# Kernel tuning notes

Measured on AMD Instinct MI355X. Metric: run time of the kernel, lower is better.

The kernel has to match this reference:

```python
import jax, jax.numpy as jnp
import numpy as np

B, L = 16, 2048          # batch, raw history length
H, S, M = 512, 8, 512    # hidden_dim, sequence_count, max_seq_len
V = 32000                # shared embed_tokens vocab
TG = 64                  # TIME_GAP_BUCKET_COUNT
LN_EPS = 1e-5


def setup_inputs() -> dict:
    key = jax.random.key(0)
    ks = jax.random.split(key, 16)
    f = lambda k, shp, scale=0.02: jax.random.normal(k, shp, jnp.float32) * scale
    return {
        "history_tokens": jax.random.randint(ks[0], (B, L), 0, V),
        "history_post_tokens": jax.random.randint(ks[1], (B, L), 0, V),
        "history_author_tokens": jax.random.randint(ks[2], (B, L), 0, V),
        "history_action_tokens": jax.random.randint(ks[3], (B, L), 0, V),
        "history_time_gap": jax.random.randint(ks[4], (B, L), 0, TG + 1),
        "history_group_ids": jax.random.randint(ks[5], (B, L), 0, S + 1),
        "history_mask": jax.random.randint(ks[6], (B, L), 0, 2).astype(bool),
        "embed_table": f(ks[7], (V, H)),
        "time_gap_table": f(ks[8], (TG + 1, H)).at[0].set(0.0),   # padding_idx=0
        "seq_id_table": f(ks[9], (S + 1, H)).at[0].set(0.0),      # padding_idx=0
        "pos_table": f(ks[10], (M, H)),
        "ln_gamma": jnp.ones((5 * H,), jnp.float32),
        "ln_beta": jnp.zeros((5 * H,), jnp.float32),
        "w1": f(ks[11], (5 * H, 4 * H)),
        "b1": jnp.zeros((4 * H,), jnp.float32),
        "w2": f(ks[12], (4 * H, H)),
        "b2": jnp.zeros((H,), jnp.float32),
        "empty_tokens": f(ks[13], (S, H)),
    }


def _forward(embed_table, time_gap_table, seq_id_table, pos_table, ln_gamma, ln_beta,
             w1, b1, w2, b2, empty_tokens,
             history_tokens, history_post_tokens, history_author_tokens,
             history_action_tokens, history_time_gap, history_group_ids, history_mask):
    # --- event feature construction: 4 shared-vocab lookups + time-gap embedding ---
    h = embed_table[history_tokens]            # [B,L,H]
    p = embed_table[history_post_tokens]
    a = embed_table[history_author_tokens]
    act = embed_table[history_action_tokens]
    gap_idx = jnp.clip(history_time_gap, 0, TG)
    gap = time_gap_table[gap_idx] * (gap_idx != 0)[..., None]  # padding_idx=0 -> zero vec
    x = jnp.concatenate([h, p, a, act, gap], axis=-1)           # [B,L,5H]

    # --- event_projection: LayerNorm -> Linear -> SiLU -> (Dropout eval) -> Linear ---
    mu = x.mean(-1, keepdims=True)
    var = x.var(-1, keepdims=True)
    xn = (x - mu) * jax.lax.rsqrt(var + LN_EPS) * ln_gamma + ln_beta
    mid = jax.nn.silu(xn @ w1 + b1)                             # [B,L,4H]
    event = mid @ w2 + b2                                       # [B,L,H]

    # --- ragged regroup: for each (b, s) gather masked positions with group id s+1,
    #     keep the LAST M of them, scatter to slots 0..count-1 ---
    gid = history_group_ids                                     # [B,L]
    match = history_mask[:, None, :] & (gid[:, None, :] == jnp.arange(1, S + 1)[None, :, None])  # [B,S,L]
    cum = jnp.cumsum(match.astype(jnp.int32), axis=-1)          # rank+1 within group
    count = cum[..., -1]                                        # [B,S]
    offset = jnp.maximum(count - M, 0)                          # drop all but last M
    slot = cum - 1 - offset[..., None]                          # [B,S,L]
    keep = match & (slot >= 0)
    slot = jnp.where(keep, slot, M)                             # M is out-of-range -> dropped

    b_idx = jnp.arange(B)[:, None, None]
    s_idx = jnp.arange(S)[None, :, None]
    states = jnp.zeros((B, S, M, H), event.dtype)
    states = states.at[b_idx, s_idx, slot].set(event[:, None, :, :], mode="drop")
    smask = jnp.zeros((B, S, M), bool)
    smask = smask.at[b_idx, s_idx, slot].set(True, mode="drop")

    # empty groups get the learned empty token at slot 0
    empty = count == 0                                          # [B,S]
    states = states.at[:, :, 0, :].set(
        jnp.where(empty[..., None], empty_tokens[None], states[:, :, 0, :]))
    smask = smask.at[:, :, 0].set(smask[:, :, 0] | empty)

    # positional + sequence-id embeddings, then zero padded slots
    pos = pos_table[None, None]                                 # [1,1,M,H]
    sid = seq_id_table[1:S + 1][None, :, None, :]               # [1,S,1,H]
    states = (states + pos + sid) * smask[..., None].astype(states.dtype)
    return states, smask


def reference(history_tokens, history_post_tokens, history_author_tokens,
              history_action_tokens, history_time_gap, history_group_ids, history_mask,
              embed_table, time_gap_table, seq_id_table, pos_table, ln_gamma, ln_beta,
              w1, b1, w2, b2, empty_tokens):
    return _forward(embed_table, time_gap_table, seq_id_table, pos_table, ln_gamma, ln_beta,
                    w1, b1, w2, b2, empty_tokens,
                    history_tokens, history_post_tokens, history_author_tokens,
                    history_action_tokens, history_time_gap, history_group_ids, history_mask)
```

## Files before the change

kernel.cpp:

```cpp
#include <hip/hip_runtime.h>
#include <hip/hip_bf16.h>
#include <stdint.h>

#define B_ 16
#define L_ 2048
#define H_ 512
#define S_ 8
#define M_ 512
#define TG_ 64
#define NTOK (B_ * L_)
#define FIVEH (5 * H_)
#define FOURH (4 * H_)

typedef __attribute__((ext_vector_type(4))) float f32x4;
typedef __attribute__((ext_vector_type(8))) short bf16x8;

__device__ __forceinline__ short f2bf(float f) {
  unsigned u = __builtin_bit_cast(unsigned, f);
  unsigned r = (u + 0x7FFFu + ((u >> 16) & 1u)) >> 16;
  return (short)r;
}

__device__ __forceinline__ void gload_lds16(const void* g, void* l) {
  __builtin_amdgcn_global_load_lds(
      (const __attribute__((address_space(1))) unsigned int*)g,
      (__attribute__((address_space(3))) unsigned int*)l, 16, 0, 0);
}


#define BAR __builtin_amdgcn_s_barrier()
#define LGKM0 do { asm volatile("s_waitcnt lgkmcnt(0)" ::: "memory"); \
                   __builtin_amdgcn_sched_barrier(0); } while (0)
#define VMW(n) asm volatile("s_waitcnt vmcnt(" #n ")" ::: "memory")
#define PRIO(p) __builtin_amdgcn_s_setprio(p)

#define STAGE(src, isB, slot, half, kt) do {                                  \
    const short* _s = (src) + (size_t)((half) * 128) * K + (kt);              \
    const int _o = ((isB) ? 65536 : 0) + (slot) * 32768 + (half) * 16384;     \
    gload_lds16(_s + (size_t)sr0 * K + sc0, lds + _o + db0);                  \
    gload_lds16(_s + (size_t)sr1 * K + sc1, lds + _o + db1);                  \
  } while (0)

#define LDA(qr, slot) do { const int _b = (slot) * 32768 + aW + (qr) * 8192;  \
    _Pragma("unroll") for (int fm = 0; fm < 4; ++fm)                          \
    _Pragma("unroll") for (int ks = 0; ks < 2; ++ks)                          \
      a[fm][ks] = *(const bf16x8*)(lds + _b + sA[fm][ks]); } while (0)

#define LDB(dst, qc, slot) do { const int _b = (slot) * 32768 + bW + (qc) * 4096; \
    _Pragma("unroll") for (int fn = 0; fn < 2; ++fn)                          \
    _Pragma("unroll") for (int ks = 0; ks < 2; ++ks)                          \
      dst[fn][ks] = *(const bf16x8*)(lds + _b + sB[fn][ks]); } while (0)

#define MFMA16(qr, qc, bs) do {                                               \
    _Pragma("unroll") for (int fm = 0; fm < 4; ++fm)                          \
    _Pragma("unroll") for (int fn = 0; fn < 2; ++fn)                          \
    _Pragma("unroll") for (int ks = 0; ks < 2; ++ks)                          \
      acc[(qr)*4+fm][(qc)*2+fn] = __builtin_amdgcn_mfma_f32_16x16x32_bf16(    \
          a[fm][ks], bs[fn][ks], acc[(qr)*4+fm][(qc)*2+fn], 0, 0, 0); } while (0)

template<int K>
__device__ __forceinline__ void gemm_core(const short* __restrict__ Ag,
                                          const short* __restrict__ Bg,
                                          char* lds, f32x4 (&acc)[8][4],
                                          int tid) {
  constexpr int NITER = K / 128;
  const int lane = tid & 63;
  const int wave = tid >> 6;
  const int wm = wave >> 2;
  const int wn = wave & 3;
  const int la = lane & 15;
  const int hi = lane >> 4;

  const int x = (la & 7) << 4;
  int sA[4][2], sB[2][2];
#pragma unroll
  for (int fm = 0; fm < 4; ++fm)
#pragma unroll
    for (int ks = 0; ks < 2; ++ks)
      sA[fm][ks] = (((fm * 16 + la) * 128) + (ks * 32 + hi * 8) * 2) ^ x;
#pragma unroll
  for (int fn = 0; fn < 2; ++fn)
#pragma unroll
    for (int ks = 0; ks < 2; ++ks)
      sB[fn][ks] = ((((wn & 1) * 64 + fn * 16 + la) * 128) + (ks * 32 + hi * 8) * 2) ^ x;
  const int aW = wm * 16384;
  const int bW = 65536 + (wn >> 1) * 16384;

  const int db0 = tid * 16, db1 = tid * 16 + 8192;
  const int lb0 = db0 ^ (((db0 >> 7) & 7) << 4);
  const int lb1 = db1 ^ (((db1 >> 7) & 7) << 4);
  const int sr0 = lb0 >> 7, sc0 = (lb0 & 127) >> 1;
  const int sr1 = lb1 >> 7, sc1 = (lb1 & 127) >> 1;

  bf16x8 a[4][2], b0v[2][2], b1v[2][2];

  STAGE(Bg, 1, 0, 0, 0); STAGE(Bg, 1, 0, 1, 0);
  STAGE(Ag, 0, 0, 0, 0); STAGE(Ag, 0, 0, 1, 0);
  STAGE(Bg, 1, 1, 0, 64); STAGE(Bg, 1, 1, 1, 64);
  VMW(0);
  BAR;

  for (int i = 0; i < NITER - 1; ++i) {
    const int kt1 = (2 * i + 1) * 64, kt2 = kt1 + 64, kt3 = kt1 + 128;
    LDA(0, 0); LDB(b0v, 0, 0); STAGE(Ag, 0, 1, 0, kt1);
    BAR; LGKM0; PRIO(1); MFMA16(0, 0, b0v); PRIO(0); BAR;
    LDB(b1v, 1, 0); STAGE(Ag, 0, 1, 1, kt1);
    BAR; LGKM0; PRIO(1); MFMA16(0, 1, b1v); PRIO(0); BAR;
    LDA(1, 0); STAGE(Bg, 1, 0, 0, kt2);
    BAR; LGKM0; PRIO(1); MFMA16(1, 1, b1v); PRIO(0); BAR;
    STAGE(Bg, 1, 0, 1, kt2);
    BAR; LGKM0; PRIO(1); MFMA16(1, 0, b0v); PRIO(0); VMW(4); BAR;
    LDA(0, 1); LDB(b0v, 0, 1); STAGE(Ag, 0, 0, 0, kt2);
    BAR; LGKM0; PRIO(1); MFMA16(0, 0, b0v); PRIO(0); BAR;
    LDB(b1v, 1, 1); STAGE(Ag, 0, 0, 1, kt2);
    BAR; LGKM0; PRIO(1); MFMA16(0, 1, b1v); PRIO(0); BAR;
    LDA(1, 1); STAGE(Bg, 1, 1, 0, kt3);
    BAR; LGKM0; PRIO(1); MFMA16(1, 1, b1v); PRIO(0); BAR;
    STAGE(Bg, 1, 1, 1, kt3);
    BAR; LGKM0; PRIO(1); MFMA16(1, 0, b0v); PRIO(0); VMW(4); BAR;
  }
  {
    const int kt1 = (2 * (NITER - 1) + 1) * 64;
    LDA(0, 0); LDB(b0v, 0, 0); STAGE(Ag, 0, 1, 0, kt1);
    BAR; LGKM0; PRIO(1); MFMA16(0, 0, b0v); PRIO(0); BAR;
    LDB(b1v, 1, 0); STAGE(Ag, 0, 1, 1, kt1);
    BAR; LGKM0; PRIO(1); MFMA16(0, 1, b1v); PRIO(0); BAR;
    LDA(1, 0);
    BAR; LGKM0; PRIO(1); MFMA16(1, 1, b1v); PRIO(0); BAR;
    BAR; LGKM0; PRIO(1); MFMA16(1, 0, b0v); PRIO(0); VMW(0); BAR;
    LDA(0, 1); LDB(b0v, 0, 1);
    BAR; LGKM0; PRIO(1); MFMA16(0, 0, b0v); PRIO(0); BAR;
    LDB(b1v, 1, 1);
    BAR; LGKM0; PRIO(1); MFMA16(0, 1, b1v); PRIO(0); BAR;
    LDA(1, 1);
    BAR; LGKM0; PRIO(1); MFMA16(1, 1, b1v); PRIO(0); BAR;
    BAR; LGKM0; PRIO(1); MFMA16(1, 0, b0v); PRIO(0);
  }
}

__global__ __launch_bounds__(512, 2) void gemm1_kernel(
    const short* __restrict__ A, const short* __restrict__ Bt,
    const float* __restrict__ bias, const int* __restrict__ nkeep,
    short* __restrict__ C) {
  const int bn = blockIdx.x & 7;
  const int bm = blockIdx.x >> 3;
  if (bm * 256 >= nkeep[0]) return;
  __shared__ __align__(16) char lds[131072];
  const int tid = threadIdx.x;
  f32x4 acc[8][4] = {};
  gemm_core<FIVEH>(A + (size_t)bm * 256 * FIVEH, Bt + (size_t)bn * 256 * FIVEH,
                   lds, acc, tid);
  const int lane = tid & 63, wave = tid >> 6;
  const int wm = wave >> 2, wn = wave & 3;
  const int la = lane & 15, hi = lane >> 4;
  const int row0 = bm * 256 + wm * 128 + hi * 4;
  const int col0 = bn * 256 + wn * 64 + la;
#pragma unroll
  for (int mi = 0; mi < 8; ++mi)
#pragma unroll
    for (int ni = 0; ni < 4; ++ni) {
      const int col = col0 + ni * 16;
      const float bv = bias[col];
#pragma unroll
      for (int r = 0; r < 4; ++r) {
        const int row = row0 + mi * 16 + r;
        float v = acc[mi][ni][r] + bv;
        float sg = 1.f / (1.f + __expf(-v));
        C[(size_t)row * FOURH + col] = f2bf(v * sg);
      }
    }
}

__global__ __launch_bounds__(512, 2) void gemm2_kernel(
    const short* __restrict__ A, const short* __restrict__ Bt,
    const float* __restrict__ b2, const float* __restrict__ pos,
    const float* __restrict__ sidtab, const int* __restrict__ destv,
    const int* __restrict__ nkeep, float* __restrict__ states) {
  const int bn = blockIdx.x & 1;
  const int bm = blockIdx.x >> 1;
  const int nk = nkeep[0];
  if (bm * 256 >= nk) return;
  __shared__ __align__(16) char lds[131072];
  const int tid = threadIdx.x;
  f32x4 acc[8][4] = {};
  gemm_core<FOURH>(A + (size_t)bm * 256 * FOURH, Bt + (size_t)bn * 256 * FOURH,
                   lds, acc, tid);
  const int lane = tid & 63, wave = tid >> 6;
  const int wm = wave >> 2, wn = wave & 3;
  const int la = lane & 15, hi = lane >> 4;
  const int row0 = bm * 256 + wm * 128 + hi * 4;
  const int col0 = bn * 256 + wn * 64 + la;
#pragma unroll
  for (int mi = 0; mi < 8; ++mi) {
#pragma unroll
    for (int r = 0; r < 4; ++r) {
      const int row = row0 + mi * 16 + r;
      if (row >= nk) continue;
      const int dest = destv[row];
      const int slot = dest & (M_ - 1);
      const int gs = dest >> 9;
      const int s = gs & (S_ - 1);
      float* orow = states + (size_t)dest * H_;
#pragma unroll
      for (int n = 0; n < 4; ++n) {
        const int col = col0 + n * 16;
        orow[col] = acc[mi][n][r] + b2[col] + pos[slot * H_ + col] +
                    sidtab[(s + 1) * H_ + col];
      }
    }
  }
}

__global__ __launch_bounds__(256) void transpose_cvt_kernel(
    const float* __restrict__ in, short* __restrict__ out, int K, int N) {
  __shared__ float tile[32][33];
  const int n0 = blockIdx.x * 32, k0 = blockIdx.y * 32;
  const int tx = threadIdx.x, ty = threadIdx.y;
#pragma unroll
  for (int i = 0; i < 32; i += 8)
    tile[ty + i][tx] = in[(size_t)(k0 + ty + i) * N + n0 + tx];
  __syncthreads();
#pragma unroll
  for (int i = 0; i < 32; i += 8)
    out[(size_t)(n0 + ty + i) * K + k0 + tx] = f2bf(tile[tx][ty + i]);
}

__global__ __launch_bounds__(256) void scan_kernel(
    const int* __restrict__ gid, const int* __restrict__ mask,
    int* __restrict__ rankv, int* __restrict__ counts) {
  const int b = blockIdx.x >> 3;
  const int s = blockIdx.x & 7;
  const int g = s + 1;
  const int base = b * L_;
  const int t = threadIdx.x;
  int loc = 0, sum = 0;
  const int l0 = t * 8;
#pragma unroll
  for (int j = 0; j < 8; ++j) {
    int l = l0 + j;
    bool mt = (mask[base + l] != 0) && (gid[base + l] == g);
    loc |= (mt ? 1 : 0) << j;
    sum += mt ? 1 : 0;
  }
  __shared__ int lds[256];
  lds[t] = sum;
  __syncthreads();
  for (int off = 1; off < 256; off <<= 1) {
    int vv = (t >= off) ? lds[t - off] : 0;
    __syncthreads();
    lds[t] += vv;
    __syncthreads();
  }
  int run = lds[t] - sum;
#pragma unroll
  for (int j = 0; j < 8; ++j) {
    if ((loc >> j) & 1) {
      run += 1;
      rankv[base + l0 + j] = run;
    }
  }
  if (t == 0) counts[blockIdx.x] = lds[255];
}

__global__ __launch_bounds__(256) void compact_kernel(
    const int* __restrict__ rankv, const int* __restrict__ counts,
    const int* __restrict__ gid, int* __restrict__ tokidx,
    int* __restrict__ destv, int* __restrict__ nkeep) {
  const int token = blockIdx.x * 256 + threadIdx.x;
  const int t = threadIdx.x;
  const int r = rankv[token];
  int dest = -1;
  if (r > 0) {
    const int g = gid[token];
    const int b = token >> 11;
    const int gs = b * S_ + (g - 1);
    const int cnt = counts[gs];
    const int over = cnt - M_;
    const int slot = r - 1 - (over > 0 ? over : 0);
    if (slot >= 0) dest = gs * M_ + slot;
  }
  const int flag = (dest >= 0) ? 1 : 0;
  __shared__ int lds[256];
  __shared__ int basep;
  lds[t] = flag;
  __syncthreads();
  for (int off = 1; off < 256; off <<= 1) {
    int vv = (t >= off) ? lds[t - off] : 0;
    __syncthreads();
    lds[t] += vv;
    __syncthreads();
  }
  if (t == 255) basep = atomicAdd(nkeep, lds[255]);
  __syncthreads();
  if (flag) {
    const int p = basep + lds[t] - 1;
    tokidx[p] = token;
    destv[p] = dest;
  }
}

__global__ __launch_bounds__(256) void gather_ln_kernel(
    const int* __restrict__ tokidx, const int* __restrict__ nkeep,
    const int* __restrict__ tok0, const int* __restrict__ tok1,
    const int* __restrict__ tok2, const int* __restrict__ tok3,
    const int* __restrict__ tgap,
    const float* __restrict__ emb, const float* __restrict__ gaptab,
    const float* __restrict__ gamma, const float* __restrict__ beta,
    short* __restrict__ xn) {
  const int wid = threadIdx.x >> 6;
  const int l = threadIdx.x & 63;
  const int j = blockIdx.x * 4 + wid;
  const int nk = nkeep[0];
  const int padded = (nk + 255) & ~255;
  if (j >= padded) return;
  short* orow = xn + (size_t)j * FIVEH;
  if (j >= nk) {
    short4 z = make_short4(0, 0, 0, 0);
#pragma unroll
    for (int i = 0; i < 10; ++i) ((short4*)orow)[i * 64 + l] = z;
    return;
  }
  const int token = tokidx[j];
  const int tk0 = tok0[token], tk1 = tok1[token], tk2 = tok2[token],
            tk3 = tok3[token];
  int gi = tgap[token];
  gi = gi < 0 ? 0 : (gi > TG_ ? TG_ : gi);
  const float4* sb[5];
  sb[0] = (const float4*)(emb + (size_t)tk0 * H_);
  sb[1] = (const float4*)(emb + (size_t)tk1 * H_);
  sb[2] = (const float4*)(emb + (size_t)tk2 * H_);
  sb[3] = (const float4*)(emb + (size_t)tk3 * H_);
  sb[4] = (const float4*)(gaptab + (size_t)gi * H_);
  float4 v[10];
  float sum = 0.f, sq = 0.f;
#pragma unroll
  for (int i = 0; i < 10; ++i) {
    const int d4 = i * 64 + l;
    const int seg = i >> 1;
    float4 x;
    if (seg < 4 || gi != 0) x = sb[seg][d4 & 127];
    else x = make_float4(0.f, 0.f, 0.f, 0.f);
    v[i] = x;
    sum += x.x + x.y + x.z + x.w;
    sq += x.x * x.x + x.y * x.y + x.z * x.z + x.w * x.w;
  }
#pragma unroll
  for (int s = 32; s; s >>= 1) {
    sum += __shfl_xor(sum, s, 64);
    sq += __shfl_xor(sq, s, 64);
  }
  const float mu = sum * (1.f / FIVEH);
  const float var = sq * (1.f / FIVEH) - mu * mu;
  const float rs = rsqrtf(var + 1e-5f);
#pragma unroll
  for (int i = 0; i < 10; ++i) {
    const int d4 = i * 64 + l;
    const float4 g4 = ((const float4*)gamma)[d4];
    const float4 b4 = ((const float4*)beta)[d4];
    short4 o;
    o.x = f2bf((v[i].x - mu) * rs * g4.x + b4.x);
    o.y = f2bf((v[i].y - mu) * rs * g4.y + b4.y);
    o.z = f2bf((v[i].z - mu) * rs * g4.z + b4.z);
    o.w = f2bf((v[i].w - mu) * rs * g4.w + b4.w);
    ((short4*)orow)[d4] = o;
  }
}

__global__ __launch_bounds__(128) void finalize_kernel(
    const int* __restrict__ counts, const float* __restrict__ empty_tok,
    const float* __restrict__ pos, const float* __restrict__ sidtab,
    float* __restrict__ states, float* __restrict__ smask) {
  const int idx = blockIdx.x;
  const int m = idx & (M_ - 1);
  const int gs = idx >> 9;
  const int s = gs & (S_ - 1);
  const int cnt = counts[gs];
  const int ce = cnt < M_ ? cnt : M_;
  const bool empty = (cnt == 0);
  const bool filled = m < ce;
  if (threadIdx.x == 0) smask[idx] = (filled || (empty && m == 0)) ? 1.0f : 0.0f;
  if (filled) return;
  float* row = states + (size_t)idx * H_;
  const int t = threadIdx.x;
  if (empty && m == 0) {
    float4 e = ((const float4*)(empty_tok + s * H_))[t];
    float4 pv = ((const float4*)pos)[t];
    float4 sd = ((const float4*)(sidtab + (s + 1) * H_))[t];
    float4 o;
    o.x = e.x + pv.x + sd.x;
    o.y = e.y + pv.y + sd.y;
    o.z = e.z + pv.z + sd.z;
    o.w = e.w + pv.w + sd.w;
    ((float4*)row)[t] = o;
  } else {
    float4 z;
    z.x = z.y = z.z = z.w = 0.f;
    ((float4*)row)[t] = z;
  }
}

extern "C" void kernel_launch(void* const* d_in, const int* in_sizes, int n_in,
                              void* d_out, int out_size, void* d_ws, size_t ws_size,
                              hipStream_t stream) {
  const int* tok0 = (const int*)d_in[0];
  const int* tok1 = (const int*)d_in[1];
  const int* tok2 = (const int*)d_in[2];
  const int* tok3 = (const int*)d_in[3];
  const int* tgap = (const int*)d_in[4];
  const int* gid = (const int*)d_in[5];
  const int* mask = (const int*)d_in[6];
  const float* emb = (const float*)d_in[7];
  const float* gaptab = (const float*)d_in[8];
  const float* sidtab = (const float*)d_in[9];
  const float* pos = (const float*)d_in[10];
  const float* gamma = (const float*)d_in[11];
  const float* beta = (const float*)d_in[12];
  const float* w1 = (const float*)d_in[13];
  const float* b1 = (const float*)d_in[14];
  const float* w2 = (const float*)d_in[15];
  const float* b2 = (const float*)d_in[16];
  const float* empty_tok = (const float*)d_in[17];

  char* p = (char*)d_ws;
  short* xn = (short*)p;  p += (size_t)NTOK * FIVEH * 2;
  short* mid = (short*)p; p += (size_t)NTOK * FOURH * 2;
  short* w1T = (short*)p; p += (size_t)FOURH * FIVEH * 2;
  short* w2T = (short*)p; p += (size_t)H_ * FOURH * 2;
  int* rankv = (int*)p;   p += (size_t)NTOK * 4;
  int* tokidx = (int*)p;  p += (size_t)NTOK * 4;
  int* destv = (int*)p;   p += (size_t)NTOK * 4;
  int* counts = (int*)p;  p += 512;
  int* nkeep = (int*)p;   p += 512;

  float* states = (float*)d_out;
  float* smask = states + (size_t)B_ * S_ * M_ * H_;

  hipMemsetAsync(rankv, 0, (size_t)NTOK * 4, stream);
  hipMemsetAsync(nkeep, 0, 4, stream);
  transpose_cvt_kernel<<<dim3(FOURH / 32, FIVEH / 32), dim3(32, 8), 0, stream>>>(
      w1, w1T, FIVEH, FOURH);
  transpose_cvt_kernel<<<dim3(H_ / 32, FOURH / 32), dim3(32, 8), 0, stream>>>(
      w2, w2T, FOURH, H_);
  scan_kernel<<<B_ * S_, 256, 0, stream>>>(gid, mask, rankv, counts);
  compact_kernel<<<NTOK / 256, 256, 0, stream>>>(rankv, counts, gid, tokidx,
                                                 destv, nkeep);
  gather_ln_kernel<<<NTOK / 4, 256, 0, stream>>>(tokidx, nkeep, tok0, tok1, tok2,
                                                 tok3, tgap, emb, gaptab, gamma,
                                                 beta, xn);
  gemm1_kernel<<<128 * 8, 512, 0, stream>>>(xn, w1T, b1, nkeep, mid);
  gemm2_kernel<<<128 * 2, 512, 0, stream>>>(mid, w2T, b2, pos, sidtab, destv,
                                            nkeep, states);
  finalize_kernel<<<B_ * S_ * M_, 128, 0, stream>>>(counts, empty_tok, pos, sidtab,
                                                    states, smask);
}
```

Before: 294.7 us.

## Retile second GEMM to 256x128 with triple-buffered LDS pipeline; grid-stride finalize

The second GEMM moves from 256x256 tiles with the shared gemm_core to 256x128 tiles, doubling the block count. It gets its own three-stage global-to-LDS pipeline with split MFMA phases and priority hints. This is meant to give better occupancy and more CUs for the K=2048 reduction, at the cost of reloading A once per extra column tile. The finalize kernel changes from one block per row to a grid-stride loop over float4 elements, which cuts the block launch count.

Measured after the change: 277.7 us. -5.7%, faster.

```diff
diff --git a/kernel.cpp b/kernel.cpp
--- a/kernel.cpp
+++ b/kernel.cpp
@@ -27,12 +27,12 @@
       (__attribute__((address_space(3))) unsigned int*)l, 16, 0, 0);
 }
 
-
 #define BAR __builtin_amdgcn_s_barrier()
 #define LGKM0 do { asm volatile("s_waitcnt lgkmcnt(0)" ::: "memory"); \
                    __builtin_amdgcn_sched_barrier(0); } while (0)
 #define VMW(n) asm volatile("s_waitcnt vmcnt(" #n ")" ::: "memory")
 #define PRIO(p) __builtin_amdgcn_s_setprio(p)
+
 
 #define STAGE(src, isB, slot, half, kt) do {                                  \
     const short* _s = (src) + (size_t)((half) * 128) * K + (kt);              \
@@ -171,27 +171,105 @@
     }
 }
 
-__global__ __launch_bounds__(512, 2) void gemm2_kernel(
+#define ASL(s) ((s) * 32768)
+#define BSL(s) (98304 + (s) * 16384)
+
+#define STG2(src, ldsoff, kt) do {                                            \
+    const short* _s = (src) + (kt);                                          \
+    gload_lds16(_s + (size_t)sr0 * 2048 + sc0, lds + (ldsoff) + db0);         \
+    gload_lds16(_s + (size_t)sr1 * 2048 + sc1, lds + (ldsoff) + db1);         \
+  } while (0)
+
+#define LDA2(slot) do { const int _b = ASL(slot) + aW2;                       \
+    _Pragma("unroll") for (int fm = 0; fm < 4; ++fm)                          \
+    _Pragma("unroll") for (int ks = 0; ks < 2; ++ks)                          \
+      a[fm][ks] = *(const bf16x8*)(lds + _b + sA2[fm][ks]); } while (0)
+
+#define LDB2a(slot) do { const int _b = BSL(slot);                            \
+    _Pragma("unroll") for (int fn = 0; fn < 2; ++fn)                          \
+    _Pragma("unroll") for (int ks = 0; ks < 2; ++ks)                          \
+      b[fn][ks] = *(const bf16x8*)(lds + _b + sB2[fn][ks]); } while (0)
+
+#define LDB2b(slot) do { const int _b = BSL(slot);                            \
+    _Pragma("unroll") for (int fn = 2; fn < 4; ++fn)                          \
+    _Pragma("unroll") for (int ks = 0; ks < 2; ++ks)                          \
+      b[fn][ks] = *(const bf16x8*)(lds + _b + sB2[fn][ks]); } while (0)
+
+#define MFMA2(h) do {                                                         \
+    _Pragma("unroll") for (int fm = 0; fm < 4; ++fm)                          \
+    _Pragma("unroll") for (int fn = 2*(h); fn < 2*(h)+2; ++fn)                \
+    _Pragma("unroll") for (int ks = 0; ks < 2; ++ks)                          \
+      acc[fm][fn] = __builtin_amdgcn_mfma_f32_16x16x32_bf16(                  \
+          a[fm][ks], b[fn][ks], acc[fm][fn], 0, 0, 0); } while (0)
+
+#define T2(slot, kt, ISSUE, WAITC) do {                                       \
+    LDA2(slot); LDB2a(slot);                                                  \
+    if (ISSUE) STG2(Ag, ASL(((slot) + 2) % 3), kt);                           \
+    BAR; LGKM0; PRIO(1); MFMA2(0); PRIO(0); BAR;                              \
+    LDB2b(slot);                                                              \
+    if (ISSUE) { STG2(Ag + 128 * 2048, ASL(((slot) + 2) % 3) + 16384, kt);    \
+                 STG2(Bg, BSL(((slot) + 2) % 3), kt); }                       \
+    BAR; LGKM0; PRIO(1); MFMA2(1); PRIO(0); WAITC; BAR;                       \
+  } while (0)
+
+__global__ __launch_bounds__(512) void gemm2_kernel(
     const short* __restrict__ A, const short* __restrict__ Bt,
     const float* __restrict__ b2, const float* __restrict__ pos,
     const float* __restrict__ sidtab, const int* __restrict__ destv,
     const int* __restrict__ nkeep, float* __restrict__ states) {
-  const int bn = blockIdx.x & 1;
-  const int bm = blockIdx.x >> 1;
+  const int bn = blockIdx.x & 3;
+  const int bm = blockIdx.x >> 2;
   const int nk = nkeep[0];
   if (bm * 256 >= nk) return;
-  __shared__ __align__(16) char lds[131072];
+  __shared__ __align__(16) char lds[147456];
   const int tid = threadIdx.x;
-  f32x4 acc[8][4] = {};
-  gemm_core<FOURH>(A + (size_t)bm * 256 * FOURH, Bt + (size_t)bn * 256 * FOURH,
-                   lds, acc, tid);
   const int lane = tid & 63, wave = tid >> 6;
-  const int wm = wave >> 2, wn = wave & 3;
+  const int wm = wave >> 1;
+  const int wn = wave & 1;
   const int la = lane & 15, hi = lane >> 4;
-  const int row0 = bm * 256 + wm * 128 + hi * 4;
-  const int col0 = bn * 256 + wn * 64 + la;
-#pragma unroll
-  for (int mi = 0; mi < 8; ++mi) {
+  const short* Ag = A + (size_t)bm * 256 * 2048;
+  const short* Bg = Bt + (size_t)bn * 128 * 2048;
+
+  const int x = (la & 7) << 4;
+  int sA2[4][2], sB2[4][2];
+#pragma unroll
+  for (int fm = 0; fm < 4; ++fm)
+#pragma unroll
+    for (int ks = 0; ks < 2; ++ks)
+      sA2[fm][ks] = ((((wm & 1) * 64 + fm * 16 + la) * 128) + (ks * 32 + hi * 8) * 2) ^ x;
+#pragma unroll
+  for (int fn = 0; fn < 4; ++fn)
+#pragma unroll
+    for (int ks = 0; ks < 2; ++ks)
+      sB2[fn][ks] = (((wn * 64 + fn * 16 + la) * 128) + (ks * 32 + hi * 8) * 2) ^ x;
+  const int aW2 = (wm >> 1) * 16384;
+
+  const int db0 = tid * 16, db1 = tid * 16 + 8192;
+  const int lb0 = db0 ^ (((db0 >> 7) & 7) << 4);
+  const int lb1 = db1 ^ (((db1 >> 7) & 7) << 4);
+  const int sr0 = lb0 >> 7, sc0 = (lb0 & 127) >> 1;
+  const int sr1 = lb1 >> 7, sc1 = (lb1 & 127) >> 1;
+
+  f32x4 acc[4][4] = {};
+  bf16x8 a[4][2], b[4][2];
+
+  STG2(Ag, ASL(0), 0); STG2(Ag + 128 * 2048, ASL(0) + 16384, 0); STG2(Bg, BSL(0), 0);
+  STG2(Ag, ASL(1), 64); STG2(Ag + 128 * 2048, ASL(1) + 16384, 64); STG2(Bg, BSL(1), 64);
+  VMW(6);
+  BAR;
+  for (int i = 0; i < 10; ++i) {
+    const int kt = i * 192 + 128;
+    T2(0, kt, true, VMW(6));
+    T2(1, kt + 64, true, VMW(6));
+    T2(2, kt + 128, true, VMW(6));
+  }
+  T2(0, 0, false, VMW(0));
+  T2(1, 0, false, ((void)0));
+
+  const int row0 = bm * 256 + wm * 64 + hi * 4;
+  const int col0 = bn * 128 + wn * 64 + la;
+#pragma unroll
+  for (int mi = 0; mi < 4; ++mi) {
 #pragma unroll
     for (int r = 0; r < 4; ++r) {
       const int row = row0 + mi * 16 + r;
@@ -337,12 +415,12 @@
   for (int i = 0; i < 10; ++i) {
     const int d4 = i * 64 + l;
     const int seg = i >> 1;
-    float4 x;
-    if (seg < 4 || gi != 0) x = sb[seg][d4 & 127];
-    else x = make_float4(0.f, 0.f, 0.f, 0.f);
-    v[i] = x;
-    sum += x.x + x.y + x.z + x.w;
-    sq += x.x * x.x + x.y * x.y + x.z * x.z + x.w * x.w;
+    float4 xv;
+    if (seg < 4 || gi != 0) xv = sb[seg][d4 & 127];
+    else xv = make_float4(0.f, 0.f, 0.f, 0.f);
+    v[i] = xv;
+    sum += xv.x + xv.y + xv.z + xv.w;
+    sq += xv.x * xv.x + xv.y * xv.y + xv.z * xv.z + xv.w * xv.w;
   }
 #pragma unroll
   for (int s = 32; s; s >>= 1) {
@@ -366,36 +444,31 @@
   }
 }
 
-__global__ __launch_bounds__(128) void finalize_kernel(
+__global__ __launch_bounds__(256) void finalize_kernel(
     const int* __restrict__ counts, const float* __restrict__ empty_tok,
     const float* __restrict__ pos, const float* __restrict__ sidtab,
     float* __restrict__ states, float* __restrict__ smask) {
-  const int idx = blockIdx.x;
-  const int m = idx & (M_ - 1);
-  const int gs = idx >> 9;
-  const int s = gs & (S_ - 1);
-  const int cnt = counts[gs];
-  const int ce = cnt < M_ ? cnt : M_;
-  const bool empty = (cnt == 0);
-  const bool filled = m < ce;
-  if (threadIdx.x == 0) smask[idx] = (filled || (empty && m == 0)) ? 1.0f : 0.0f;
-  if (filled) return;
-  float* row = states + (size_t)idx * H_;
-  const int t = threadIdx.x;
-  if (empty && m == 0) {
-    float4 e = ((const float4*)(empty_tok + s * H_))[t];
-    float4 pv = ((const float4*)pos)[t];
-    float4 sd = ((const float4*)(sidtab + (s + 1) * H_))[t];
-    float4 o;
-    o.x = e.x + pv.x + sd.x;
-    o.y = e.y + pv.y + sd.y;
-    o.z = e.z + pv.z + sd.z;
-    o.w = e.w + pv.w + sd.w;
-    ((float4*)row)[t] = o;
-  } else {
-    float4 z;
-    z.x = z.y = z.z = z.w = 0.f;
-    ((float4*)row)[t] = z;
+  const int total = B_ * S_ * M_ * (H_ / 4);
+  for (int idx = blockIdx.x * 256 + threadIdx.x; idx < total;
+       idx += gridDim.x * 256) {
+    const int row = idx >> 7, c = idx & 127;
+    const int gs = row >> 9, m = row & (M_ - 1), s = gs & (S_ - 1);
+    const int cnt = counts[gs];
+    const bool empty = (cnt == 0);
+    const bool filled = m < (cnt < M_ ? cnt : M_);
+    if (c == 0) smask[row] = (filled || (empty && m == 0)) ? 1.0f : 0.0f;
+    if (filled) continue;
+    float4 o = make_float4(0.f, 0.f, 0.f, 0.f);
+    if (empty && m == 0) {
+      float4 e = ((const float4*)(empty_tok + s * H_))[c];
+      float4 pv = ((const float4*)pos)[c];
+      float4 sd = ((const float4*)(sidtab + (s + 1) * H_))[c];
+      o.x = e.x + pv.x + sd.x;
+      o.y = e.y + pv.y + sd.y;
+      o.z = e.z + pv.z + sd.z;
+      o.w = e.w + pv.w + sd.w;
+    }
+    ((float4*)(states + (size_t)row * H_))[c] = o;
   }
 }
 
@@ -448,8 +521,8 @@
                                                  tok3, tgap, emb, gaptab, gamma,
                                                  beta, xn);
   gemm1_kernel<<<128 * 8, 512, 0, stream>>>(xn, w1T, b1, nkeep, mid);
-  gemm2_kernel<<<128 * 2, 512, 0, stream>>>(mid, w2T, b2, pos, sidtab, destv,
+  gemm2_kernel<<<128 * 4, 512, 0, stream>>>(mid, w2T, b2, pos, sidtab, destv,
                                             nkeep, states);
-  finalize_kernel<<<B_ * S_ * M_, 128, 0, stream>>>(counts, empty_tok, pos, sidtab,
-                                                    states, smask);
-}
+  finalize_kernel<<<2048, 256, 0, stream>>>(counts, empty_tok, pos, sidtab,
+                                            states, smask);
+}
```
